# Optimization experiments

Hardware: AMD Instinct MI355X
Metric: run time of the kernel (lower is better)

The kernel has to match this reference:

```python
import jax, jax.numpy as jnp
import numpy as np
from jax import lax

B, CIN, COUT, H, W = 4, 256, 256, 64, 64
K = 3  # kernel size
PAD = 1
STRIDE = 1


def setup_inputs() -> dict:
    key = jax.random.key(0)
    k1, k2, k3, k4 = jax.random.split(key, 4)
    x = jax.random.normal(k1, (B, CIN, H, W), dtype=jnp.float32)
    # small offset weights so learned offsets are modest (original init is zeros)
    offset_w = jax.random.normal(k2, (3 * K * K, CIN, K, K), dtype=jnp.float32) * 0.01
    offset_b = jax.random.normal(k3, (3 * K * K,), dtype=jnp.float32) * 0.01
    dcn_w = jax.random.normal(k4, (COUT, CIN, K, K), dtype=jnp.float32) * (1.0 / np.sqrt(CIN * K * K))
    return {"x": x, "offset_w": offset_w, "offset_b": offset_b, "dcn_w": dcn_w}


def _dcnv2(x, offset_w, offset_b, dcn_w):
    b, c, h, w = x.shape
    kk = K * K
    # offset conv (standard 3x3, stride 1, pad 1)
    o = lax.conv_general_dilated(
        x, offset_w, (STRIDE, STRIDE), ((PAD, PAD), (PAD, PAD)),
        dimension_numbers=("NCHW", "OIHW", "NCHW"))
    o = o + offset_b[None, :, None, None]
    ho, wo = o.shape[2], o.shape[3]
    off = o[:, : 2 * kk].reshape(b, kk, 2, ho, wo)  # pairs are (dy, dx)
    dy, dx = off[:, :, 0], off[:, :, 1]             # [b,kk,ho,wo]
    mask = jax.nn.sigmoid(o[:, 2 * kk:])            # [b,kk,ho,wo]

    ki, kj = jnp.meshgrid(jnp.arange(K), jnp.arange(K), indexing="ij")
    ki = ki.reshape(kk).astype(jnp.float32)
    kj = kj.reshape(kk).astype(jnp.float32)
    base_y = (jnp.arange(ho, dtype=jnp.float32) * STRIDE - PAD)[None, None, :, None] + ki[None, :, None, None]
    base_x = (jnp.arange(wo, dtype=jnp.float32) * STRIDE - PAD)[None, None, None, :] + kj[None, :, None, None]
    py = base_y + dy  # [b,kk,ho,wo] sampling y
    px = base_x + dx  # sampling x

    y0 = jnp.floor(py)
    x0 = jnp.floor(px)
    wy = py - y0  # bilinear fractional weights
    wx = px - x0
    y0i = y0.astype(jnp.int32)
    x0i = x0.astype(jnp.int32)

    xT = x.transpose(0, 2, 3, 1)  # [b,h,w,c] for channel-last gathers
    bidx = jnp.arange(b)[:, None, None, None]

    def gather(yi, xi):
        # zero padding outside the image
        valid = (yi >= 0) & (yi < h) & (xi >= 0) & (xi < w)
        yc = jnp.clip(yi, 0, h - 1)
        xc = jnp.clip(xi, 0, w - 1)
        v = xT[bidx, yc, xc]  # [b,kk,ho,wo,c]
        return v * valid[..., None].astype(x.dtype)

    g00 = gather(y0i, x0i)
    g01 = gather(y0i, x0i + 1)
    g10 = gather(y0i + 1, x0i)
    g11 = gather(y0i + 1, x0i + 1)

    wy_ = wy[..., None]
    wx_ = wx[..., None]
    sampled = (g00 * (1 - wy_) * (1 - wx_) + g01 * (1 - wy_) * wx_
               + g10 * wy_ * (1 - wx_) + g11 * wy_ * wx_)
    sampled = sampled * mask[..., None]  # modulation

    wk = dcn_w.reshape(dcn_w.shape[0], c, kk)  # [o,c,kk]
    return jnp.einsum("bkhwc,ock->bohw", sampled, wk)


def reference(x, offset_w, offset_b, dcn_w):
    return _dcnv2(x, offset_w, offset_b, dcn_w)
```

## Files before the change

kernel.cpp:

```cpp
#include <hip/hip_runtime.h>
#include <hip/hip_bf16.h>
#include <stdint.h>
#include <math.h>

#define KDIM 2304

typedef __attribute__((ext_vector_type(8))) short bf16x8;
typedef __attribute__((ext_vector_type(4))) float f32x4;

__device__ inline unsigned short f2bf(float f) {
  union { float f; unsigned int u; } v; v.f = f;
  unsigned int u = v.u;
  unsigned int r = (u + 0x7FFFu + ((u >> 16) & 1u)) >> 16;
  return (unsigned short)r;
}
__device__ inline float bf2f(unsigned short h) {
  union { unsigned int u; float f; } v; v.u = ((unsigned int)h) << 16;
  return v.f;
}

__device__ inline void gl2lds16(const void* g, void* l) {
  __builtin_amdgcn_global_load_lds((const __attribute__((address_space(1))) void*)g,
                                   (__attribute__((address_space(3))) void*)l,
                                   16, 0, 0);
}

__global__ __launch_bounds__(256) void k_transpose(const float* __restrict__ x,
                                                   unsigned short* __restrict__ xTb) {
  __shared__ float tile[32][33];
  int t = threadIdx.x;
  int tx = t & 31, ty = t >> 5;
  int p0 = blockIdx.x * 32;
  int c0 = blockIdx.y * 32;
  int b  = blockIdx.z;
  const float* xb = x + ((size_t)b << 20);
#pragma unroll
  for (int i = 0; i < 4; ++i) {
    int c = c0 + ty + i * 8;
    tile[ty + i * 8][tx] = xb[((size_t)c << 12) + p0 + tx];
  }
  __syncthreads();
  unsigned short* ob = xTb + ((size_t)b << 20);
#pragma unroll
  for (int i = 0; i < 4; ++i) {
    int p = p0 + ty + i * 8;
    ob[(((size_t)p) << 8) + c0 + tx] = f2bf(tile[tx][ty + i * 8]);
  }
}

__global__ __launch_bounds__(256) void k_wprep(const float* __restrict__ dcn_w,
                                               const float* __restrict__ offset_w,
                                               unsigned short* __restrict__ Wpk,
                                               unsigned short* __restrict__ Wob,
                                               unsigned short* __restrict__ zp) {
  int gid = blockIdx.x * 256 + threadIdx.x;
  const int N1 = 72 * 8192;
  const int N2 = 32 * KDIM;
  if (gid < N1) {
    int j = gid & 7;
    int lane = (gid >> 3) & 63;
    int mb = (gid >> 9) & 15;
    int kc = gid >> 13;
    int row = mb * 16 + (lane & 15);
    int gk = kc * 32 + ((lane >> 4) << 3) + j;
    int c = gk & 255, kidx = gk >> 8;
    Wpk[gid] = f2bf(dcn_w[((size_t)(row * 256 + c)) * 9 + kidx]);
  } else if (gid < N1 + N2) {
    int g = gid - N1;
    int ch = g / KDIM, k = g % KDIM;
    int kidx = k >> 8, c = k & 255;
    Wob[g] = (ch < 27) ? f2bf(offset_w[((size_t)(ch * 256 + c)) * 9 + kidx])
                       : (unsigned short)0;
  } else if (gid < N1 + N2 + 128) {
    zp[gid - N1 - N2] = 0;
  }
}

__global__ __launch_bounds__(256) void k_offs_gemm(const unsigned short* __restrict__ xTb,
                                                   const unsigned short* __restrict__ Wob,
                                                   const unsigned short* __restrict__ zp,
                                                   float* __restrict__ O2p) {
  __shared__ unsigned short As[2][64 * 32];
  __shared__ unsigned short Bs[2][32 * 32];
  int t = threadIdx.x;
  int wv = t >> 6, lane = t & 63;
  int bid = (int)blockIdx.x;
  int swz = (bid & 7) * 32 + (bid >> 3);
  int n0 = swz * 64;
  int z = blockIdx.y;
  int r0 = t >> 2, coff = (t & 3) * 8;

  int rowA = n0 + r0;
  int b_ = rowA >> 12, hw = rowA & 4095, h = hw >> 6, w = hw & 63;

  f32x4 acc[2] = {};

  auto stage = [&](int kt, int buf) {
    int k0 = kt * 32;
    int kidx = k0 >> 8, c0 = k0 & 255;
    int di = kidx / 3 - 1, dj = kidx % 3 - 1;
    int y = h + di, xx = w + dj;
    const unsigned short* g = (y >= 0 && y < 64 && xx >= 0 && xx < 64)
        ? xTb + (((((size_t)b_) << 12) + (y << 6) + xx) << 8) + c0 + coff
        : zp;
    gl2lds16(g, (char*)As[buf] + wv * 1024);
    if (t < 128) {
      const unsigned short* gB = Wob + (size_t)(t >> 2) * KDIM + k0 + coff;
      gl2lds16(gB, (char*)Bs[buf] + wv * 1024);
    }
  };

  int kbeg = z * 36, kend = kbeg + 36;
  stage(kbeg, 0);

  for (int kt = kbeg; kt < kend; ++kt) {
    int buf = (kt - kbeg) & 1;
    if (kt + 1 < kend) {
      stage(kt + 1, buf ^ 1);
      if (wv < 2) asm volatile("s_waitcnt vmcnt(2)" ::: "memory");
      else        asm volatile("s_waitcnt vmcnt(1)" ::: "memory");
    } else {
      asm volatile("s_waitcnt vmcnt(0)" ::: "memory");
    }
    asm volatile("s_barrier" ::: "memory");

    bf16x8 aF, bF[2];
    aF = *(const bf16x8*)(As[buf] + (wv * 16 + (lane & 15)) * 32 + (lane >> 4) * 8);
#pragma unroll
    for (int j = 0; j < 2; ++j)
      bF[j] = *(const bf16x8*)(Bs[buf] + (j * 16 + (lane & 15)) * 32 + (lane >> 4) * 8);
#pragma unroll
    for (int j = 0; j < 2; ++j)
      acc[j] = __builtin_amdgcn_mfma_f32_16x16x32_bf16(aF, bF[j], acc[j], 0, 0, 0);

    asm volatile("s_barrier" ::: "memory");
  }

  int quad = lane >> 4, cl = lane & 15;
  float* O2z = O2p + (size_t)z * 16384 * 32;
#pragma unroll
  for (int j = 0; j < 2; ++j) {
    int col = j * 16 + cl;
#pragma unroll
    for (int r = 0; r < 4; ++r) {
      int row = n0 + wv * 16 + quad * 4 + r;
      O2z[(size_t)row * 32 + col] = acc[j][r];
    }
  }
}

__global__ __launch_bounds__(256) void k_sweights(const float* __restrict__ O2p,
                                                  const float* __restrict__ offb,
                                                  float* __restrict__ SW) {
  int gid = blockIdx.x * 256 + threadIdx.x;
  if (gid >= 9 * 16384) return;
  int k = gid >> 14;
  int bhw = gid & 16383;
  int h = (bhw >> 6) & 63, w = bhw & 63;

  const float* o0 = O2p + (size_t)bhw * 32;
  const float* o1 = o0 + (size_t)16384 * 32;
  float dy = o0[2 * k]     + o1[2 * k]     + offb[2 * k];
  float dx = o0[2 * k + 1] + o1[2 * k + 1] + offb[2 * k + 1];
  float mv = o0[18 + k]    + o1[18 + k]    + offb[18 + k];
  float mask = 1.0f / (1.0f + expf(-mv));

  float py = (float)(h - 1 + k / 3) + dy;
  float px = (float)(w - 1 + k % 3) + dx;
  float y0f = floorf(py), x0f = floorf(px);
  float wy = py - y0f, wx = px - x0f;
  int y0 = (int)y0f, x0 = (int)x0f;
  int y1 = y0 + 1, x1 = x0 + 1;

  float vy0 = (y0 >= 0 && y0 < 64) ? 1.f : 0.f;
  float vy1 = (y1 >= 0 && y1 < 64) ? 1.f : 0.f;
  float vx0 = (x0 >= 0 && x0 < 64) ? 1.f : 0.f;
  float vx1 = (x1 >= 0 && x1 < 64) ? 1.f : 0.f;
  int y0c = min(max(y0, 0), 63), y1c = min(max(y1, 0), 63);
  int x0c = min(max(x0, 0), 63), x1c = min(max(x1, 0), 63);

  float4 wv4;
  wv4.x = (1.f - wy) * (1.f - wx) * vy0 * vx0 * mask;
  wv4.y = (1.f - wy) * wx * vy0 * vx1 * mask;
  wv4.z = wy * (1.f - wx) * vy1 * vx0 * mask;
  wv4.w = wy * wx * vy1 * vx1 * mask;
  uint4 ov;
  ov.x = (unsigned)(((y0c << 6) + x0c) << 8);
  ov.y = (unsigned)(((y0c << 6) + x1c) << 8);
  ov.z = (unsigned)(((y1c << 6) + x0c) << 8);
  ov.w = (unsigned)(((y1c << 6) + x1c) << 8);

  float* p = SW + (size_t)gid * 8;
  *(float4*)p = wv4;
  *(uint4*)(p + 4) = ov;
}

#define FSTEP(KT, Q, AF, BUF, DOSW)                                            \
  do {                                                                         \
    float s0_ = wv4.x * bf2f(Q[0].x) + wv4.y * bf2f(Q[1].x) +                  \
                wv4.z * bf2f(Q[2].x) + wv4.w * bf2f(Q[3].x);                   \
    float s1_ = wv4.x * bf2f(Q[0].y) + wv4.y * bf2f(Q[1].y) +                  \
                wv4.z * bf2f(Q[2].y) + wv4.w * bf2f(Q[3].y);                   \
    float s2_ = wv4.x * bf2f(Q[0].z) + wv4.y * bf2f(Q[1].z) +                  \
                wv4.z * bf2f(Q[2].z) + wv4.w * bf2f(Q[3].z);                   \
    float s3_ = wv4.x * bf2f(Q[0].w) + wv4.y * bf2f(Q[1].w) +                  \
                wv4.z * bf2f(Q[2].w) + wv4.w * bf2f(Q[3].w);                   \
    union { __hip_bfloat162 h2[2]; ushort4 v; } pk_;                           \
    pk_.h2[0] = __float22bfloat162_rn(make_float2(s0_, s1_));                  \
    pk_.h2[1] = __float22bfloat162_rn(make_float2(s2_, s3_));                  \
    *(ushort4*)(&Bs[BUF][bsw]) = pk_.v;                                        \
    if (DOSW && ((KT) & 7) == 0 && (KT) < 64) {                                \
      const float* swp_ =                                                      \
          SW + ((size_t)(((((KT) >> 3) + 1) << 14) + n0 + r)) * 8;             \
      wv4n = *(const float4*)swp_;                                             \
      ovn  = *(const uint4*)(swp_ + 4);                                        \
    }                                                                          \
    if ((KT) < 70) {                                                           \
      int kn_ = (KT) + 2;                                                      \
      uint4 o_ = (((KT) & 7) >= 6) ? ovn : ov;                                 \
      unsigned c_ = (unsigned)(((kn_ & 7) << 5) + ch0);                        \
      Q[0] = *(const ushort4*)(xb + o_.x + c_);                                \
      Q[1] = *(const ushort4*)(xb + o_.y + c_);                                \
      Q[2] = *(const ushort4*)(xb + o_.z + c_);                                \
      Q[3] = *(const ushort4*)(xb + o_.w + c_);                                \
    }                                                                          \
    asm volatile("s_waitcnt lgkmcnt(0)\n\ts_barrier" ::: "memory");            \
    bf16x8 bF0_ = *(const bf16x8*)(&Bs[BUF][(wn * 32 + (lane & 15)) * 40 +     \
                                            (lane >> 4) * 8]);                 \
    bf16x8 bF1_ = *(const bf16x8*)(&Bs[BUF][(wn * 32 + 16 + (lane & 15)) * 40 +\
                                            (lane >> 4) * 8]);                 \
    _Pragma("unroll")                                                          \
    for (int i_ = 0; i_ < 4; ++i_) {                                           \
      acc[i_][0] =                                                             \
          __builtin_amdgcn_mfma_f32_16x16x32_bf16(AF[i_], bF0_, acc[i_][0],    \
                                                  0, 0, 0);                    \
      acc[i_][1] =                                                             \
          __builtin_amdgcn_mfma_f32_16x16x32_bf16(AF[i_], bF1_, acc[i_][1],    \
                                                  0, 0, 0);                    \
    }                                                                          \
    if ((KT) < 70) {                                                           \
      int kn_ = (KT) + 2;                                                      \
      _Pragma("unroll")                                                        \
      for (int i_ = 0; i_ < 4; ++i_)                                           \
        AF[i_] = *(const bf16x8*)(wpBase + ((size_t)kn_ * 16 + i_) * 512);     \
    }                                                                          \
  } while (0)

__global__ __launch_bounds__(512) void k_fused(const unsigned short* __restrict__ Wpk,
                                               const unsigned short* __restrict__ xTb,
                                               const float* __restrict__ SW,
                                               float* __restrict__ out) {
  __shared__ __align__(16) unsigned short Bs[2][64 * 40];
  int t = threadIdx.x;
  int wv = t >> 6, lane = t & 63;
  int wm = wv & 3, wn = wv >> 2;
  int bid = (int)blockIdx.x;
  int swz = (bid & 7) * 32 + (bid >> 3);
  int n0 = swz * 64;
  int b  = n0 >> 12;
  const unsigned short* xb = xTb + ((size_t)b << 20);

  int r = t >> 3, g = t & 7;
  int ch0 = g * 4;
  int bsw = r * 40 + ch0;

  const unsigned short* wpBase = Wpk + ((size_t)(wm * 4 * 64 + lane)) * 8;

  f32x4 acc[4][2] = {};

  float4 wv4, wv4n; uint4 ov, ovn;
  {
    const float* sw = SW + ((size_t)(n0 + r)) * 8;
    wv4 = *(const float4*)sw;
    ov  = *(const uint4*)(sw + 4);
  }
  wv4n = wv4; ovn = ov;

  ushort4 qA[4], qB[4];
  bf16x8 aFA[4], aFB[4];

  {
    unsigned c0_ = (unsigned)ch0;
    qA[0] = *(const ushort4*)(xb + ov.x + c0_);
    qA[1] = *(const ushort4*)(xb + ov.y + c0_);
    qA[2] = *(const ushort4*)(xb + ov.z + c0_);
    qA[3] = *(const ushort4*)(xb + ov.w + c0_);
    unsigned c1_ = (unsigned)(32 + ch0);
    qB[0] = *(const ushort4*)(xb + ov.x + c1_);
    qB[1] = *(const ushort4*)(xb + ov.y + c1_);
    qB[2] = *(const ushort4*)(xb + ov.z + c1_);
    qB[3] = *(const ushort4*)(xb + ov.w + c1_);
#pragma unroll
    for (int i = 0; i < 4; ++i) {
      aFA[i] = *(const bf16x8*)(wpBase + (size_t)i * 512);
      aFB[i] = *(const bf16x8*)(wpBase + (size_t)(16 + i) * 512);
    }
  }

  for (int kt = 0; kt < 72; kt += 2) {
    FSTEP(kt,     qA, aFA, 0, 1);
    FSTEP(kt + 1, qB, aFB, 1, 0);
    if ((kt & 7) == 6) { wv4 = wv4n; ov = ovn; }
  }

  int quad = lane >> 4, cl = lane & 15;
  float* ob = out + (((size_t)b) << 20);
#pragma unroll
  for (int i = 0; i < 4; ++i) {
    int mbase = wm * 64 + i * 16 + quad * 4;
#pragma unroll
    for (int j = 0; j < 2; ++j) {
      int hw = (n0 & 4095) + wn * 32 + j * 16 + cl;
      float* op = ob + hw;
#pragma unroll
      for (int rr = 0; rr < 4; ++rr)
        op[((size_t)(mbase + rr)) << 12] = acc[i][j][rr];
    }
  }
}

extern "C" void kernel_launch(void* const* d_in, const int* in_sizes, int n_in,
                              void* d_out, int out_size, void* d_ws, size_t ws_size,
                              hipStream_t stream) {
  const float* x        = (const float*)d_in[0];
  const float* offset_w = (const float*)d_in[1];
  const float* offset_b = (const float*)d_in[2];
  const float* dcn_w    = (const float*)d_in[3];
  float* out = (float*)d_out;

  char* ws = (char*)d_ws;
  size_t off = 0;
  auto carve = [&](size_t bytes) -> void* {
    void* p = ws + off;
    off += (bytes + 255) & ~(size_t)255;
    return p;
  };
  unsigned short* xTb = (unsigned short*)carve(4ull * 64 * 64 * 256 * 2);
  unsigned short* Wpk = (unsigned short*)carve(72ull * 8192 * 2);
  unsigned short* Wob = (unsigned short*)carve(32ull * KDIM * 2);
  unsigned short* zp  = (unsigned short*)carve(256);
  float*          O2p = (float*)carve(2ull * 16384 * 32 * 4);
  float*          SW  = (float*)carve(9ull * 16384 * 8 * 4);
  (void)ws_size; (void)in_sizes; (void)n_in; (void)out_size;

  k_transpose<<<dim3(128, 8, 4), 256, 0, stream>>>(x, xTb);
  k_wprep<<<dim3((72 * 8192 + 32 * KDIM + 128 + 255) / 256), 256, 0, stream>>>(
      dcn_w, offset_w, Wpk, Wob, zp);
  k_offs_gemm<<<dim3(256, 2), 256, 0, stream>>>(xTb, Wob, zp, O2p);
  k_sweights<<<dim3((9 * 16384 + 255) / 256), 256, 0, stream>>>(O2p, offset_b, SW);
  k_fused<<<dim3(256), 512, 0, stream>>>(Wpk, xTb, SW, out);
}
```

Measured before the change: 149.6 us.

## Halve fused-kernel N tile to 32 and stage offset sums in LDS

The fused deformable-conv GEMM moves from 64-column to 32-column tiles, doubling the grid to 512 blocks. Each of the 8 waves now covers 32 output rows, and only the first 256 threads do the bilinear sampling. This is meant to fill more CUs and cut accumulator registers, at the cost of reloading the weight fragments twice as often and leaving half the threads idle during sampling. Separately, the sampling-weight kernel now loads both partial offset-conv outputs with coalesced float4 reads into shared memory before computing per-tap weights, replacing strided scalar reads.

After: 149.6 us. No clear change (-0.0%).

```diff
diff --git a/kernel.cpp b/kernel.cpp
--- a/kernel.cpp
+++ b/kernel.cpp
@@ -152,85 +152,98 @@
 __global__ __launch_bounds__(256) void k_sweights(const float* __restrict__ O2p,
                                                   const float* __restrict__ offb,
                                                   float* __restrict__ SW) {
-  int gid = blockIdx.x * 256 + threadIdx.x;
-  if (gid >= 9 * 16384) return;
-  int k = gid >> 14;
-  int bhw = gid & 16383;
-  int h = (bhw >> 6) & 63, w = bhw & 63;
-
-  const float* o0 = O2p + (size_t)bhw * 32;
-  const float* o1 = o0 + (size_t)16384 * 32;
-  float dy = o0[2 * k]     + o1[2 * k]     + offb[2 * k];
-  float dx = o0[2 * k + 1] + o1[2 * k + 1] + offb[2 * k + 1];
-  float mv = o0[18 + k]    + o1[18 + k]    + offb[18 + k];
-  float mask = 1.0f / (1.0f + expf(-mv));
-
-  float py = (float)(h - 1 + k / 3) + dy;
-  float px = (float)(w - 1 + k % 3) + dx;
-  float y0f = floorf(py), x0f = floorf(px);
-  float wy = py - y0f, wx = px - x0f;
-  int y0 = (int)y0f, x0 = (int)x0f;
-  int y1 = y0 + 1, x1 = x0 + 1;
-
-  float vy0 = (y0 >= 0 && y0 < 64) ? 1.f : 0.f;
-  float vy1 = (y1 >= 0 && y1 < 64) ? 1.f : 0.f;
-  float vx0 = (x0 >= 0 && x0 < 64) ? 1.f : 0.f;
-  float vx1 = (x1 >= 0 && x1 < 64) ? 1.f : 0.f;
-  int y0c = min(max(y0, 0), 63), y1c = min(max(y1, 0), 63);
-  int x0c = min(max(x0, 0), 63), x1c = min(max(x1, 0), 63);
-
-  float4 wv4;
-  wv4.x = (1.f - wy) * (1.f - wx) * vy0 * vx0 * mask;
-  wv4.y = (1.f - wy) * wx * vy0 * vx1 * mask;
-  wv4.z = wy * (1.f - wx) * vy1 * vx0 * mask;
-  wv4.w = wy * wx * vy1 * vx1 * mask;
-  uint4 ov;
-  ov.x = (unsigned)(((y0c << 6) + x0c) << 8);
-  ov.y = (unsigned)(((y0c << 6) + x1c) << 8);
-  ov.z = (unsigned)(((y1c << 6) + x0c) << 8);
-  ov.w = (unsigned)(((y1c << 6) + x1c) << 8);
-
-  float* p = SW + (size_t)gid * 8;
-  *(float4*)p = wv4;
-  *(uint4*)(p + 4) = ov;
+  __shared__ float os[32][33];
+  int t = threadIdx.x;
+  int bhw0 = blockIdx.x * 32;
+  {
+    int row = t >> 3, c4 = t & 7;
+    const float4* p0 = (const float4*)(O2p + (size_t)(bhw0 + row) * 32) + c4;
+    const float4* p1 = (const float4*)(O2p + (size_t)(16384 + bhw0 + row) * 32) + c4;
+    float4 a = *p0, b = *p1;
+    os[row][c4 * 4 + 0] = a.x + b.x;
+    os[row][c4 * 4 + 1] = a.y + b.y;
+    os[row][c4 * 4 + 2] = a.z + b.z;
+    os[row][c4 * 4 + 3] = a.w + b.w;
+  }
+  __syncthreads();
+  for (int item = t; item < 288; item += 256) {
+    int bl = item & 31, k = item >> 5;
+    int bhw = bhw0 + bl;
+    int h = (bhw >> 6) & 63, w = bhw & 63;
+    float dy = os[bl][2 * k]     + offb[2 * k];
+    float dx = os[bl][2 * k + 1] + offb[2 * k + 1];
+    float mv = os[bl][18 + k]    + offb[18 + k];
+    float mask = 1.0f / (1.0f + expf(-mv));
+
+    float py = (float)(h - 1 + k / 3) + dy;
+    float px = (float)(w - 1 + k % 3) + dx;
+    float y0f = floorf(py), x0f = floorf(px);
+    float wy = py - y0f, wx = px - x0f;
+    int y0 = (int)y0f, x0 = (int)x0f;
+    int y1 = y0 + 1, x1 = x0 + 1;
+
+    float vy0 = (y0 >= 0 && y0 < 64) ? 1.f : 0.f;
+    float vy1 = (y1 >= 0 && y1 < 64) ? 1.f : 0.f;
+    float vx0 = (x0 >= 0 && x0 < 64) ? 1.f : 0.f;
+    float vx1 = (x1 >= 0 && x1 < 64) ? 1.f : 0.f;
+    int y0c = min(max(y0, 0), 63), y1c = min(max(y1, 0), 63);
+    int x0c = min(max(x0, 0), 63), x1c = min(max(x1, 0), 63);
+
+    float4 wv4;
+    wv4.x = (1.f - wy) * (1.f - wx) * vy0 * vx0 * mask;
+    wv4.y = (1.f - wy) * wx * vy0 * vx1 * mask;
+    wv4.z = wy * (1.f - wx) * vy1 * vx0 * mask;
+    wv4.w = wy * wx * vy1 * vx1 * mask;
+    uint4 ov;
+    ov.x = (unsigned)(((y0c << 6) + x0c) << 8);
+    ov.y = (unsigned)(((y0c << 6) + x1c) << 8);
+    ov.z = (unsigned)(((y1c << 6) + x0c) << 8);
+    ov.w = (unsigned)(((y1c << 6) + x1c) << 8);
+
+    float* p = SW + (size_t)(k * 16384 + bhw) * 8;
+    *(float4*)p = wv4;
+    *(uint4*)(p + 4) = ov;
+  }
 }
 
 #define FSTEP(KT, Q, AF, BUF, DOSW)                                            \
   do {                                                                         \
-    float s0_ = wv4.x * bf2f(Q[0].x) + wv4.y * bf2f(Q[1].x) +                  \
-                wv4.z * bf2f(Q[2].x) + wv4.w * bf2f(Q[3].x);                   \
-    float s1_ = wv4.x * bf2f(Q[0].y) + wv4.y * bf2f(Q[1].y) +                  \
-                wv4.z * bf2f(Q[2].y) + wv4.w * bf2f(Q[3].y);                   \
-    float s2_ = wv4.x * bf2f(Q[0].z) + wv4.y * bf2f(Q[1].z) +                  \
-                wv4.z * bf2f(Q[2].z) + wv4.w * bf2f(Q[3].z);                   \
-    float s3_ = wv4.x * bf2f(Q[0].w) + wv4.y * bf2f(Q[1].w) +                  \
-                wv4.z * bf2f(Q[2].w) + wv4.w * bf2f(Q[3].w);                   \
-    union { __hip_bfloat162 h2[2]; ushort4 v; } pk_;                           \
-    pk_.h2[0] = __float22bfloat162_rn(make_float2(s0_, s1_));                  \
-    pk_.h2[1] = __float22bfloat162_rn(make_float2(s2_, s3_));                  \
-    *(ushort4*)(&Bs[BUF][bsw]) = pk_.v;                                        \
-    if (DOSW && ((KT) & 7) == 0 && (KT) < 64) {                                \
-      const float* swp_ =                                                      \
-          SW + ((size_t)(((((KT) >> 3) + 1) << 14) + n0 + r)) * 8;             \
-      wv4n = *(const float4*)swp_;                                             \
-      ovn  = *(const uint4*)(swp_ + 4);                                        \
-    }                                                                          \
-    if ((KT) < 70) {                                                           \
-      int kn_ = (KT) + 2;                                                      \
-      uint4 o_ = (((KT) & 7) >= 6) ? ovn : ov;                                 \
-      unsigned c_ = (unsigned)(((kn_ & 7) << 5) + ch0);                        \
-      Q[0] = *(const ushort4*)(xb + o_.x + c_);                                \
-      Q[1] = *(const ushort4*)(xb + o_.y + c_);                                \
-      Q[2] = *(const ushort4*)(xb + o_.z + c_);                                \
-      Q[3] = *(const ushort4*)(xb + o_.w + c_);                                \
+    if (t < 256) {                                                             \
+      float s0_ = wv4.x * bf2f(Q[0].x) + wv4.y * bf2f(Q[1].x) +                \
+                  wv4.z * bf2f(Q[2].x) + wv4.w * bf2f(Q[3].x);                 \
+      float s1_ = wv4.x * bf2f(Q[0].y) + wv4.y * bf2f(Q[1].y) +                \
+                  wv4.z * bf2f(Q[2].y) + wv4.w * bf2f(Q[3].y);                 \
+      float s2_ = wv4.x * bf2f(Q[0].z) + wv4.y * bf2f(Q[1].z) +                \
+                  wv4.z * bf2f(Q[2].z) + wv4.w * bf2f(Q[3].z);                 \
+      float s3_ = wv4.x * bf2f(Q[0].w) + wv4.y * bf2f(Q[1].w) +                \
+                  wv4.z * bf2f(Q[2].w) + wv4.w * bf2f(Q[3].w);                 \
+      union { __hip_bfloat162 h2[2]; ushort4 v; } pk_;                         \
+      pk_.h2[0] = __float22bfloat162_rn(make_float2(s0_, s1_));                \
+      pk_.h2[1] = __float22bfloat162_rn(make_float2(s2_, s3_));                \
+      *(ushort4*)(&Bs[BUF][bsw]) = pk_.v;                                      \
+      if (DOSW && ((KT) & 7) == 0 && (KT) < 64) {                              \
+        const float* swp_ =                                                    \
+            SW + ((size_t)(((((KT) >> 3) + 1) << 14) + n0 + r)) * 8;           \
+        wv4n = *(const float4*)swp_;                                           \
+        ovn  = *(const uint4*)(swp_ + 4);                                      \
+      }                                                                        \
+      if ((KT) < 70) {                                                         \
+        int kn_ = (KT) + 2;                                                    \
+        uint4 o_ = (((KT) & 7) >= 6) ? ovn : ov;                               \
+        unsigned c_ = (unsigned)(((kn_ & 7) << 5) + ch0);                      \
+        Q[0] = *(const ushort4*)(xb + o_.x + c_);                              \
+        Q[1] = *(const ushort4*)(xb + o_.y + c_);                              \
+        Q[2] = *(const ushort4*)(xb + o_.z + c_);                              \
+        Q[3] = *(const ushort4*)(xb + o_.w + c_);                              \
+      }                                                                        \
     }                                                                          \
     asm volatile("s_waitcnt lgkmcnt(0)\n\ts_barrier" ::: "memory");            \
-    bf16x8 bF0_ = *(const bf16x8*)(&Bs[BUF][(wn * 32 + (lane & 15)) * 40 +     \
+    bf16x8 bF0_ = *(const bf16x8*)(&Bs[BUF][((lane & 15)) * 40 +               \
                                             (lane >> 4) * 8]);                 \
-    bf16x8 bF1_ = *(const bf16x8*)(&Bs[BUF][(wn * 32 + 16 + (lane & 15)) * 40 +\
+    bf16x8 bF1_ = *(const bf16x8*)(&Bs[BUF][(16 + (lane & 15)) * 40 +          \
                                             (lane >> 4) * 8]);                 \
     _Pragma("unroll")                                                          \
-    for (int i_ = 0; i_ < 4; ++i_) {                                           \
+    for (int i_ = 0; i_ < 2; ++i_) {                                           \
       acc[i_][0] =                                                             \
           __builtin_amdgcn_mfma_f32_16x16x32_bf16(AF[i_], bF0_, acc[i_][0],    \
                                                   0, 0, 0);                    \
@@ -241,45 +254,42 @@
     if ((KT) < 70) {                                                           \
       int kn_ = (KT) + 2;                                                      \
       _Pragma("unroll")                                                        \
-      for (int i_ = 0; i_ < 4; ++i_)                                           \
-        AF[i_] = *(const bf16x8*)(wpBase + ((size_t)kn_ * 16 + i_) * 512);     \
+      for (int i_ = 0; i_ < 2; ++i_)                                           \
+        AF[i_] = *(const bf16x8*)(wpBase + ((size_t)(kn_ * 16 + i_)) * 512);   \
     }                                                                          \
   } while (0)
 
-__global__ __launch_bounds__(512) void k_fused(const unsigned short* __restrict__ Wpk,
-                                               const unsigned short* __restrict__ xTb,
-                                               const float* __restrict__ SW,
-                                               float* __restrict__ out) {
-  __shared__ __align__(16) unsigned short Bs[2][64 * 40];
+__global__ __launch_bounds__(512, 4) void k_fused(const unsigned short* __restrict__ Wpk,
+                                                  const unsigned short* __restrict__ xTb,
+                                                  const float* __restrict__ SW,
+                                                  float* __restrict__ out) {
+  __shared__ __align__(16) unsigned short Bs[2][32 * 40];
   int t = threadIdx.x;
   int wv = t >> 6, lane = t & 63;
-  int wm = wv & 3, wn = wv >> 2;
+  int wm = wv;
   int bid = (int)blockIdx.x;
-  int swz = (bid & 7) * 32 + (bid >> 3);
-  int n0 = swz * 64;
+  int n0 = ((bid & 7) * 64 + (bid >> 3)) * 32;
   int b  = n0 >> 12;
   const unsigned short* xb = xTb + ((size_t)b << 20);
 
-  int r = t >> 3, g = t & 7;
+  int r = (t & 255) >> 3, g = t & 7;
   int ch0 = g * 4;
   int bsw = r * 40 + ch0;
 
-  const unsigned short* wpBase = Wpk + ((size_t)(wm * 4 * 64 + lane)) * 8;
-
-  f32x4 acc[4][2] = {};
-
-  float4 wv4, wv4n; uint4 ov, ovn;
-  {
+  const unsigned short* wpBase = Wpk + (size_t)(wm * 2) * 512 + (size_t)lane * 8;
+
+  f32x4 acc[2][2] = {};
+
+  float4 wv4 = {}, wv4n = {};
+  uint4 ov = {}, ovn = {};
+  ushort4 qA[4] = {}, qB[4] = {};
+  bf16x8 aFA[2], aFB[2];
+
+  if (t < 256) {
     const float* sw = SW + ((size_t)(n0 + r)) * 8;
     wv4 = *(const float4*)sw;
     ov  = *(const uint4*)(sw + 4);
-  }
-  wv4n = wv4; ovn = ov;
-
-  ushort4 qA[4], qB[4];
-  bf16x8 aFA[4], aFB[4];
-
-  {
+    wv4n = wv4; ovn = ov;
     unsigned c0_ = (unsigned)ch0;
     qA[0] = *(const ushort4*)(xb + ov.x + c0_);
     qA[1] = *(const ushort4*)(xb + ov.y + c0_);
@@ -290,27 +300,27 @@
     qB[1] = *(const ushort4*)(xb + ov.y + c1_);
     qB[2] = *(const ushort4*)(xb + ov.z + c1_);
     qB[3] = *(const ushort4*)(xb + ov.w + c1_);
-#pragma unroll
-    for (int i = 0; i < 4; ++i) {
-      aFA[i] = *(const bf16x8*)(wpBase + (size_t)i * 512);
-      aFB[i] = *(const bf16x8*)(wpBase + (size_t)(16 + i) * 512);
-    }
+  }
+#pragma unroll
+  for (int i = 0; i < 2; ++i) {
+    aFA[i] = *(const bf16x8*)(wpBase + (size_t)i * 512);
+    aFB[i] = *(const bf16x8*)(wpBase + (size_t)(16 + i) * 512);
   }
 
   for (int kt = 0; kt < 72; kt += 2) {
     FSTEP(kt,     qA, aFA, 0, 1);
     FSTEP(kt + 1, qB, aFB, 1, 0);
-    if ((kt & 7) == 6) { wv4 = wv4n; ov = ovn; }
+    if (t < 256 && (kt & 7) == 6) { wv4 = wv4n; ov = ovn; }
   }
 
   int quad = lane >> 4, cl = lane & 15;
   float* ob = out + (((size_t)b) << 20);
 #pragma unroll
-  for (int i = 0; i < 4; ++i) {
-    int mbase = wm * 64 + i * 16 + quad * 4;
+  for (int i = 0; i < 2; ++i) {
+    int mbase = wm * 32 + i * 16 + quad * 4;
 #pragma unroll
     for (int j = 0; j < 2; ++j) {
-      int hw = (n0 & 4095) + wn * 32 + j * 16 + cl;
+      int hw = (n0 & 4095) + j * 16 + cl;
       float* op = ob + hw;
 #pragma unroll
       for (int rr = 0; rr < 4; ++rr)
@@ -347,6 +357,6 @@
   k_wprep<<<dim3((72 * 8192 + 32 * KDIM + 128 + 255) / 256), 256, 0, stream>>>(
       dcn_w, offset_w, Wpk, Wob, zp);
   k_offs_gemm<<<dim3(256, 2), 256, 0, stream>>>(xTb, Wob, zp, O2p);
-  k_sweights<<<dim3((9 * 16384 + 255) / 256), 256, 0, stream>>>(O2p, offset_b, SW);
-  k_fused<<<dim3(256), 512, 0, stream>>>(Wpk, xTb, SW, out);
-}
+  k_sweights<<<dim3(512), 256, 0, stream>>>(O2p, offset_b, SW);
+  k_fused<<<dim3(512), 512, 0, stream>>>(Wpk, xTb, SW, out);
+}
```

## Merge prep kernels and fuse offset GEMM with sampling-weight computation

Applied to the files above, without the earlier changes.

Combines the input transpose and weight-prep kernels into one launch. The offset-conv GEMM drops its 2-way K split: it now runs 512 threads over all 72 K-steps, keeps the result tile in LDS, and computes the bilinear sampling weights and gather offsets in the same kernel. This removes two launches, the partial-sum buffer round-trip through global memory and its reduction. In exchange there is half the block-level parallelism in the offset GEMM (256 blocks) and a longer serial K loop per block.

Result: no change. 147.8 us (-1.2%).

```diff
diff --git a/kernel.cpp b/kernel.cpp
--- a/kernel.cpp
+++ b/kernel.cpp
@@ -25,174 +25,161 @@
                                    16, 0, 0);
 }
 
-__global__ __launch_bounds__(256) void k_transpose(const float* __restrict__ x,
-                                                   unsigned short* __restrict__ xTb) {
+__global__ __launch_bounds__(256) void k_prep(const float* __restrict__ x,
+                                              unsigned short* __restrict__ xTb,
+                                              const float* __restrict__ dcn_w,
+                                              const float* __restrict__ offset_w,
+                                              unsigned short* __restrict__ Wpk,
+                                              unsigned short* __restrict__ Wob,
+                                              unsigned short* __restrict__ zp) {
   __shared__ float tile[32][33];
+  int bx = (int)blockIdx.x;
   int t = threadIdx.x;
-  int tx = t & 31, ty = t >> 5;
-  int p0 = blockIdx.x * 32;
-  int c0 = blockIdx.y * 32;
-  int b  = blockIdx.z;
-  const float* xb = x + ((size_t)b << 20);
-#pragma unroll
-  for (int i = 0; i < 4; ++i) {
-    int c = c0 + ty + i * 8;
-    tile[ty + i * 8][tx] = xb[((size_t)c << 12) + p0 + tx];
-  }
-  __syncthreads();
-  unsigned short* ob = xTb + ((size_t)b << 20);
-#pragma unroll
-  for (int i = 0; i < 4; ++i) {
-    int p = p0 + ty + i * 8;
-    ob[(((size_t)p) << 8) + c0 + tx] = f2bf(tile[tx][ty + i * 8]);
-  }
-}
-
-__global__ __launch_bounds__(256) void k_wprep(const float* __restrict__ dcn_w,
-                                               const float* __restrict__ offset_w,
-                                               unsigned short* __restrict__ Wpk,
-                                               unsigned short* __restrict__ Wob,
-                                               unsigned short* __restrict__ zp) {
-  int gid = blockIdx.x * 256 + threadIdx.x;
-  const int N1 = 72 * 8192;
-  const int N2 = 32 * KDIM;
-  if (gid < N1) {
-    int j = gid & 7;
-    int lane = (gid >> 3) & 63;
-    int mb = (gid >> 9) & 15;
-    int kc = gid >> 13;
-    int row = mb * 16 + (lane & 15);
-    int gk = kc * 32 + ((lane >> 4) << 3) + j;
-    int c = gk & 255, kidx = gk >> 8;
-    Wpk[gid] = f2bf(dcn_w[((size_t)(row * 256 + c)) * 9 + kidx]);
-  } else if (gid < N1 + N2) {
-    int g = gid - N1;
-    int ch = g / KDIM, k = g % KDIM;
-    int kidx = k >> 8, c = k & 255;
-    Wob[g] = (ch < 27) ? f2bf(offset_w[((size_t)(ch * 256 + c)) * 9 + kidx])
-                       : (unsigned short)0;
-  } else if (gid < N1 + N2 + 128) {
-    zp[gid - N1 - N2] = 0;
-  }
-}
-
-__global__ __launch_bounds__(256) void k_offs_gemm(const unsigned short* __restrict__ xTb,
-                                                   const unsigned short* __restrict__ Wob,
-                                                   const unsigned short* __restrict__ zp,
-                                                   float* __restrict__ O2p) {
+  if (bx < 4096) {
+    int tx = t & 31, ty = t >> 5;
+    int p0 = (bx & 127) * 32;
+    int c0 = ((bx >> 7) & 7) * 32;
+    int b  = bx >> 10;
+    const float* xb = x + ((size_t)b << 20);
+#pragma unroll
+    for (int i = 0; i < 4; ++i) {
+      int c = c0 + ty + i * 8;
+      tile[ty + i * 8][tx] = xb[((size_t)c << 12) + p0 + tx];
+    }
+    __syncthreads();
+    unsigned short* ob = xTb + ((size_t)b << 20);
+#pragma unroll
+    for (int i = 0; i < 4; ++i) {
+      int p = p0 + ty + i * 8;
+      ob[(((size_t)p) << 8) + c0 + tx] = f2bf(tile[tx][ty + i * 8]);
+    }
+  } else {
+    int gid = (bx - 4096) * 256 + t;
+    const int N1 = 72 * 8192;
+    const int N2 = 32 * KDIM;
+    if (gid < N1) {
+      int j = gid & 7;
+      int lane = (gid >> 3) & 63;
+      int mb = (gid >> 9) & 15;
+      int kc = gid >> 13;
+      int row = mb * 16 + (lane & 15);
+      int gk = kc * 32 + ((lane >> 4) << 3) + j;
+      int c = gk & 255, kidx = gk >> 8;
+      Wpk[gid] = f2bf(dcn_w[((size_t)(row * 256 + c)) * 9 + kidx]);
+    } else if (gid < N1 + N2) {
+      int g = gid - N1;
+      int ch = g / KDIM, k = g % KDIM;
+      int kidx = k >> 8, c = k & 255;
+      Wob[g] = (ch < 27) ? f2bf(offset_w[((size_t)(ch * 256 + c)) * 9 + kidx])
+                         : (unsigned short)0;
+    } else if (gid < N1 + N2 + 128) {
+      zp[gid - N1 - N2] = 0;
+    }
+  }
+}
+
+__global__ __launch_bounds__(512) void k_offs(const unsigned short* __restrict__ xTb,
+                                              const unsigned short* __restrict__ Wob,
+                                              const unsigned short* __restrict__ zp,
+                                              const float* __restrict__ offb,
+                                              float* __restrict__ SW) {
   __shared__ unsigned short As[2][64 * 32];
   __shared__ unsigned short Bs[2][32 * 32];
+  __shared__ float Os[64][33];
   int t = threadIdx.x;
   int wv = t >> 6, lane = t & 63;
   int bid = (int)blockIdx.x;
   int swz = (bid & 7) * 32 + (bid >> 3);
   int n0 = swz * 64;
-  int z = blockIdx.y;
   int r0 = t >> 2, coff = (t & 3) * 8;
 
-  int rowA = n0 + r0;
+  int rowA = n0 + (r0 & 63);
   int b_ = rowA >> 12, hw = rowA & 4095, h = hw >> 6, w = hw & 63;
 
-  f32x4 acc[2] = {};
+  f32x4 acc = {};
 
   auto stage = [&](int kt, int buf) {
     int k0 = kt * 32;
     int kidx = k0 >> 8, c0 = k0 & 255;
-    int di = kidx / 3 - 1, dj = kidx % 3 - 1;
-    int y = h + di, xx = w + dj;
-    const unsigned short* g = (y >= 0 && y < 64 && xx >= 0 && xx < 64)
-        ? xTb + (((((size_t)b_) << 12) + (y << 6) + xx) << 8) + c0 + coff
-        : zp;
-    gl2lds16(g, (char*)As[buf] + wv * 1024);
-    if (t < 128) {
-      const unsigned short* gB = Wob + (size_t)(t >> 2) * KDIM + k0 + coff;
-      gl2lds16(gB, (char*)Bs[buf] + wv * 1024);
+    if (t < 256) {
+      int di = kidx / 3 - 1, dj = kidx % 3 - 1;
+      int y = h + di, xx = w + dj;
+      const unsigned short* g = (y >= 0 && y < 64 && xx >= 0 && xx < 64)
+          ? xTb + (((((size_t)b_) << 12) + (y << 6) + xx) << 8) + c0 + coff
+          : zp;
+      gl2lds16(g, (char*)As[buf] + wv * 1024);
+    } else if (t < 384) {
+      int tt = t - 256;
+      const unsigned short* gB = Wob + (size_t)(tt >> 2) * KDIM + k0 + (tt & 3) * 8;
+      gl2lds16(gB, (char*)Bs[buf] + (wv - 4) * 1024);
     }
   };
 
-  int kbeg = z * 36, kend = kbeg + 36;
-  stage(kbeg, 0);
-
-  for (int kt = kbeg; kt < kend; ++kt) {
-    int buf = (kt - kbeg) & 1;
-    if (kt + 1 < kend) {
+  stage(0, 0);
+
+  int mf = wv & 3, nf = wv >> 2;
+  for (int kt = 0; kt < 72; ++kt) {
+    int buf = kt & 1;
+    if (kt + 1 < 72) {
       stage(kt + 1, buf ^ 1);
-      if (wv < 2) asm volatile("s_waitcnt vmcnt(2)" ::: "memory");
-      else        asm volatile("s_waitcnt vmcnt(1)" ::: "memory");
+      if (t < 384) asm volatile("s_waitcnt vmcnt(1)" ::: "memory");
+      else         asm volatile("s_waitcnt vmcnt(0)" ::: "memory");
     } else {
       asm volatile("s_waitcnt vmcnt(0)" ::: "memory");
     }
     asm volatile("s_barrier" ::: "memory");
 
-    bf16x8 aF, bF[2];
-    aF = *(const bf16x8*)(As[buf] + (wv * 16 + (lane & 15)) * 32 + (lane >> 4) * 8);
-#pragma unroll
-    for (int j = 0; j < 2; ++j)
-      bF[j] = *(const bf16x8*)(Bs[buf] + (j * 16 + (lane & 15)) * 32 + (lane >> 4) * 8);
-#pragma unroll
-    for (int j = 0; j < 2; ++j)
-      acc[j] = __builtin_amdgcn_mfma_f32_16x16x32_bf16(aF, bF[j], acc[j], 0, 0, 0);
+    bf16x8 aF = *(const bf16x8*)(As[buf] + (mf * 16 + (lane & 15)) * 32 + (lane >> 4) * 8);
+    bf16x8 bF = *(const bf16x8*)(Bs[buf] + (nf * 16 + (lane & 15)) * 32 + (lane >> 4) * 8);
+    acc = __builtin_amdgcn_mfma_f32_16x16x32_bf16(aF, bF, acc, 0, 0, 0);
 
     asm volatile("s_barrier" ::: "memory");
   }
 
   int quad = lane >> 4, cl = lane & 15;
-  float* O2z = O2p + (size_t)z * 16384 * 32;
-#pragma unroll
-  for (int j = 0; j < 2; ++j) {
-    int col = j * 16 + cl;
-#pragma unroll
-    for (int r = 0; r < 4; ++r) {
-      int row = n0 + wv * 16 + quad * 4 + r;
-      O2z[(size_t)row * 32 + col] = acc[j][r];
-    }
-  }
-}
-
-__global__ __launch_bounds__(256) void k_sweights(const float* __restrict__ O2p,
-                                                  const float* __restrict__ offb,
-                                                  float* __restrict__ SW) {
-  int gid = blockIdx.x * 256 + threadIdx.x;
-  if (gid >= 9 * 16384) return;
-  int k = gid >> 14;
-  int bhw = gid & 16383;
-  int h = (bhw >> 6) & 63, w = bhw & 63;
-
-  const float* o0 = O2p + (size_t)bhw * 32;
-  const float* o1 = o0 + (size_t)16384 * 32;
-  float dy = o0[2 * k]     + o1[2 * k]     + offb[2 * k];
-  float dx = o0[2 * k + 1] + o1[2 * k + 1] + offb[2 * k + 1];
-  float mv = o0[18 + k]    + o1[18 + k]    + offb[18 + k];
-  float mask = 1.0f / (1.0f + expf(-mv));
-
-  float py = (float)(h - 1 + k / 3) + dy;
-  float px = (float)(w - 1 + k % 3) + dx;
-  float y0f = floorf(py), x0f = floorf(px);
-  float wy = py - y0f, wx = px - x0f;
-  int y0 = (int)y0f, x0 = (int)x0f;
-  int y1 = y0 + 1, x1 = x0 + 1;
-
-  float vy0 = (y0 >= 0 && y0 < 64) ? 1.f : 0.f;
-  float vy1 = (y1 >= 0 && y1 < 64) ? 1.f : 0.f;
-  float vx0 = (x0 >= 0 && x0 < 64) ? 1.f : 0.f;
-  float vx1 = (x1 >= 0 && x1 < 64) ? 1.f : 0.f;
-  int y0c = min(max(y0, 0), 63), y1c = min(max(y1, 0), 63);
-  int x0c = min(max(x0, 0), 63), x1c = min(max(x1, 0), 63);
-
-  float4 wv4;
-  wv4.x = (1.f - wy) * (1.f - wx) * vy0 * vx0 * mask;
-  wv4.y = (1.f - wy) * wx * vy0 * vx1 * mask;
-  wv4.z = wy * (1.f - wx) * vy1 * vx0 * mask;
-  wv4.w = wy * wx * vy1 * vx1 * mask;
-  uint4 ov;
-  ov.x = (unsigned)(((y0c << 6) + x0c) << 8);
-  ov.y = (unsigned)(((y0c << 6) + x1c) << 8);
-  ov.z = (unsigned)(((y1c << 6) + x0c) << 8);
-  ov.w = (unsigned)(((y1c << 6) + x1c) << 8);
-
-  float* p = SW + (size_t)gid * 8;
-  *(float4*)p = wv4;
-  *(uint4*)(p + 4) = ov;
+#pragma unroll
+  for (int r = 0; r < 4; ++r)
+    Os[mf * 16 + quad * 4 + r][nf * 16 + cl] = acc[r];
+  __syncthreads();
+
+  for (int item = t; item < 576; item += 512) {
+    int bl = item & 63, k = item >> 6;
+    int bhw = n0 + bl;
+    int h_ = (bhw >> 6) & 63, w_ = bhw & 63;
+    float dy = Os[bl][2 * k]     + offb[2 * k];
+    float dx = Os[bl][2 * k + 1] + offb[2 * k + 1];
+    float mv = Os[bl][18 + k]    + offb[18 + k];
+    float mask = 1.0f / (1.0f + expf(-mv));
+
+    float py = (float)(h_ - 1 + k / 3) + dy;
+    float px = (float)(w_ - 1 + k % 3) + dx;
+    float y0f = floorf(py), x0f = floorf(px);
+    float wy = py - y0f, wx = px - x0f;
+    int y0 = (int)y0f, x0 = (int)x0f;
+    int y1 = y0 + 1, x1 = x0 + 1;
+
+    float vy0 = (y0 >= 0 && y0 < 64) ? 1.f : 0.f;
+    float vy1 = (y1 >= 0 && y1 < 64) ? 1.f : 0.f;
+    float vx0 = (x0 >= 0 && x0 < 64) ? 1.f : 0.f;
+    float vx1 = (x1 >= 0 && x1 < 64) ? 1.f : 0.f;
+    int y0c = min(max(y0, 0), 63), y1c = min(max(y1, 0), 63);
+    int x0c = min(max(x0, 0), 63), x1c = min(max(x1, 0), 63);
+
+    float4 wv4;
+    wv4.x = (1.f - wy) * (1.f - wx) * vy0 * vx0 * mask;
+    wv4.y = (1.f - wy) * wx * vy0 * vx1 * mask;
+    wv4.z = wy * (1.f - wx) * vy1 * vx0 * mask;
+    wv4.w = wy * wx * vy1 * vx1 * mask;
+    uint4 ov;
+    ov.x = (unsigned)(((y0c << 6) + x0c) << 8);
+    ov.y = (unsigned)(((y0c << 6) + x1c) << 8);
+    ov.z = (unsigned)(((y1c << 6) + x0c) << 8);
+    ov.w = (unsigned)(((y1c << 6) + x1c) << 8);
+
+    float* p = SW + (size_t)(k * 16384 + bhw) * 8;
+    *(float4*)p = wv4;
+    *(uint4*)(p + 4) = ov;
+  }
 }
 
 #define FSTEP(KT, Q, AF, BUF, DOSW)                                            \
@@ -339,14 +326,12 @@
   unsigned short* Wpk = (unsigned short*)carve(72ull * 8192 * 2);
   unsigned short* Wob = (unsigned short*)carve(32ull * KDIM * 2);
   unsigned short* zp  = (unsigned short*)carve(256);
-  float*          O2p = (float*)carve(2ull * 16384 * 32 * 4);
   float*          SW  = (float*)carve(9ull * 16384 * 8 * 4);
   (void)ws_size; (void)in_sizes; (void)n_in; (void)out_size;
 
-  k_transpose<<<dim3(128, 8, 4), 256, 0, stream>>>(x, xTb);
-  k_wprep<<<dim3((72 * 8192 + 32 * KDIM + 128 + 255) / 256), 256, 0, stream>>>(
-      dcn_w, offset_w, Wpk, Wob, zp);
-  k_offs_gemm<<<dim3(256, 2), 256, 0, stream>>>(xTb, Wob, zp, O2p);
-  k_sweights<<<dim3((9 * 16384 + 255) / 256), 256, 0, stream>>>(O2p, offset_b, SW);
+  const int WPREP_BLOCKS = (72 * 8192 + 32 * KDIM + 128 + 255) / 256;
+  k_prep<<<dim3(4096 + WPREP_BLOCKS), 256, 0, stream>>>(
+      x, xTb, dcn_w, offset_w, Wpk, Wob, zp);
+  k_offs<<<dim3(256), 512, 0, stream>>>(xTb, Wob, zp, offset_b, SW);
   k_fused<<<dim3(256), 512, 0, stream>>>(Wpk, xTb, SW, out);
 }
```
